# Optimization experiments

Measured on AMD Instinct MI355X. Metric: run time of the kernel, lower is better.

Reference implementation:

```python
import jax, jax.numpy as jnp
import numpy as np
from jax import lax

NEG = -1e9
B, H, C, TX, TY = 4, 256, 80, 256, 1024  # batch, hidden, mel bins, text len, mel len


def setup_inputs() -> dict:
    key = jax.random.key(0)
    k = jax.random.split(key, 6)
    en = jax.random.normal(k[0], (B, H, TX), jnp.float32)
    mu = jax.random.normal(k[1], (B, C, TX), jnp.float32)
    log_sigma = 0.1 * jax.random.normal(k[2], (B, C, TX), jnp.float32)
    y = jax.random.normal(k[3], (B, C, TY), jnp.float32)
    x_lengths = jax.random.randint(k[4], (B,), TX // 2, TX + 1, jnp.int32)
    y_lengths = jax.random.randint(k[5], (B,), TY // 2, TY + 1, jnp.int32)
    return {"en": en, "mu": mu, "log_sigma": log_sigma, "y": y,
            "x_lengths": x_lengths, "y_lengths": y_lengths}


def sequence_mask(lengths, max_len):
    return jnp.arange(max_len)[None, :] < lengths[:, None]


def compute_log_probs(mu, log_sigma, y):
    # y: [B,C,Ty] -> [B,1,Ty,C]; mu/log_sigma: [B,C,Tx] -> [B,Tx,1,C]
    yb = jnp.transpose(y, (0, 2, 1))[:, None]
    mub = jnp.transpose(mu, (0, 2, 1))[:, :, None]
    lsb = jnp.transpose(log_sigma, (0, 2, 1))[:, :, None]
    # mse / sigma^2 = (y-mu)^2 * exp(-2*log_sigma); mean over channel dim
    expo = -0.5 * jnp.mean((yb - mub) ** 2 * jnp.exp(-2.0 * lsb), axis=-1)  # [B,Tx,Ty]
    return expo - 0.5 * jnp.mean(lsb, axis=-1)  # broadcast [B,Tx,1] -> [B,Tx,Ty]


def maximum_path(logp, mask, x_lengths, y_lengths):
    """Monotonic alignment search (Glow-TTS Viterbi DP), vectorized over batch."""
    b, tx, ty = logp.shape
    lp = jnp.where(mask > 0, logp, NEG)
    cols = jnp.moveaxis(lp, 2, 0)  # [Ty, B, Tx]
    v0 = jnp.broadcast_to(jnp.where(jnp.arange(tx) == 0, 0.0, NEG), (b, tx)).astype(logp.dtype)

    def fwd(v, col):
        v_shift = jnp.concatenate([jnp.full((b, 1), NEG, v.dtype), v[:, :-1]], axis=1)
        diag = v_shift > v  # come from (x-1, y-1) rather than (x, y-1)
        return col + jnp.maximum(v, v_shift), diag

    _, diags = lax.scan(fwd, v0, cols)  # diags: [Ty, B, Tx] bool

    xs_idx = jnp.arange(tx)

    def bwd(idx, inp):
        yv, dcol = inp
        active = yv < y_lengths  # [B]
        row = (xs_idx[None, :] == idx[:, None]) & active[:, None]
        d = jnp.take_along_axis(dcol, idx[:, None], axis=1)[:, 0]
        idx = jnp.where(active & (idx > 0) & d, idx - 1, idx)
        return idx, row

    _, rows = lax.scan(bwd, x_lengths - 1, (jnp.arange(ty), diags), reverse=True)
    return lax.stop_gradient(jnp.moveaxis(rows, 0, 2).astype(logp.dtype))  # [B,Tx,Ty]


def generate_path(dr, mask):
    # dr: [B,Tx] durations; mask: [B,Tx,Ty]
    ty = mask.shape[-1]
    cum = jnp.cumsum(dr, axis=1)
    pm = (jnp.arange(ty)[None, None, :] < cum[:, :, None]).astype(dr.dtype)
    path = pm - jnp.pad(pm, ((0, 0), (1, 0), (0, 0)))[:, :-1]
    return path * mask


def reference(en, mu, log_sigma, y, x_lengths, y_lengths):
    tx, ty = mu.shape[-1], y.shape[-1]
    x_mask = sequence_mask(x_lengths, tx).astype(jnp.float32)  # [B,Tx]
    y_mask = sequence_mask(y_lengths, ty).astype(jnp.float32)  # [B,Ty]
    attn_mask = x_mask[:, :, None] * y_mask[:, None, :]        # [B,Tx,Ty]
    logp = compute_log_probs(mu, log_sigma, y)
    attn = maximum_path(logp, attn_mask, x_lengths, y_lengths)
    dr_mas = jnp.sum(attn, axis=-1)                            # durations [B,Tx]
    path = generate_path(dr_mas, attn_mask)                    # convert_dr_to_align
    # expand_encoder_outputs: attn^T @ en^T -> [B,H,Ty]
    o_en_ex = jnp.einsum('bxy,bhx->bhy', path, en)
    return o_en_ex, logp, attn, dr_mas
```

## Files before the change

### kernel.cpp

```cpp
#include <hip/hip_runtime.h>
#include <cstdint>
#include <cmath>

#define B_ 4
#define H_ 256
#define C_ 80
#define TX_ 256
#define TY_ 1024
#define NEGF (-1e9f)

#define OFF_LOGP (B_*H_*TY_)
#define OFF_ATTN (OFF_LOGP + B_*TX_*TY_)
#define OFF_DR   (OFF_ATTN + B_*TX_*TY_)

__global__ __launch_bounds__(256) void k_logp(
    const float* __restrict__ mu, const float* __restrict__ ls,
    const float* __restrict__ y, const int* __restrict__ xlp,
    const int* __restrict__ ylp, float* __restrict__ logp_out,
    float* __restrict__ lpT)
{
  const int b  = blockIdx.z;
  const int tq = blockIdx.y;
  const int x0 = blockIdx.x * 4;
  const int tid = threadIdx.x;
  const int lane = tid & 63;
  const int xi = tid >> 6;

  __shared__ double2 s_wm[4][C_];
  __shared__ double  s_wm2[4][C_];
  __shared__ double  s_lsv[4][C_];
  __shared__ double  s_K[4];
  __shared__ double  s_t0[4];
  __shared__ float   tile[256][4];

  for (int i = tid; i < 4 * C_; i += 256) {
    int xj = i / C_, c = i - xj * C_;
    double m = (double)mu[(b * C_ + c) * TX_ + x0 + xj];
    double l = (double)ls[(b * C_ + c) * TX_ + x0 + xj];
    double w = exp(-2.0 * l);
    s_wm[xj][c]  = make_double2(w, -2.0 * w * m);
    s_wm2[xj][c] = w * m * m;
    s_lsv[xj][c] = l;
  }
  __syncthreads();
  {
    int cc = lane;
    double kp = (cc < C_) ? s_wm2[xi][cc] : 0.0;
    double tp = (cc < C_) ? s_lsv[xi][cc] : 0.0;
    if (cc + 64 < C_) { kp += s_wm2[xi][cc + 64]; tp += s_lsv[xi][cc + 64]; }
#pragma unroll
    for (int off = 32; off; off >>= 1) {
      kp += __shfl_down(kp, off);
      tp += __shfl_down(tp, off);
    }
    if (cc == 0) { s_K[xi] = kp; s_t0[xi] = -0.5 * (tp * (1.0 / C_)); }
  }
  __syncthreads();

  double acc[4];
#pragma unroll
  for (int k = 0; k < 4; ++k) acc[k] = 0.0;

  const float4* yp = (const float4*)(y + (size_t)b * C_ * TY_ + tq * 256) + lane;
#pragma unroll 4
  for (int c = 0; c < C_; ++c) {
    float4 yv = yp[c * (TY_ / 4)];
    double y0 = yv.x, y1 = yv.y, y2 = yv.z, y3 = yv.w;
    double2 wm = s_wm[xi][c];
    double w = wm.x, m1 = wm.y;
    double u0 = fma(w, y0, m1), u1 = fma(w, y1, m1);
    double u2 = fma(w, y2, m1), u3 = fma(w, y3, m1);
    acc[0] = fma(u0, y0, acc[0]);
    acc[1] = fma(u1, y1, acc[1]);
    acc[2] = fma(u2, y2, acc[2]);
    acc[3] = fma(u3, y3, acc[3]);
  }

  const int xlen = xlp[b], ylen = ylp[b];
  const int x  = x0 + xi;
  const int t0 = tq * 256 + lane * 4;
  {
    double c0 = s_t0[xi], K = s_K[xi];
    float r[4];
#pragma unroll
    for (int k = 0; k < 4; ++k)
      r[k] = (float)((acc[k] + K) * (-0.5 / C_) + c0);
    *(float4*)&logp_out[((size_t)(b * TX_ + x)) * TY_ + t0] =
        make_float4(r[0], r[1], r[2], r[3]);
    bool xm = x < xlen;
#pragma unroll
    for (int k = 0; k < 4; ++k)
      tile[lane * 4 + k][xi] = (xm && (t0 + k) < ylen) ? r[k] : NEGF;
  }
  __syncthreads();

  float* dst = lpT + (size_t)b * TY_ * TX_ + x0;
  const float4* tp = (const float4*)tile;
  *(float4*)&dst[(size_t)(tq * 256 + tid) * TX_] = tp[tid];
}

#define POLL_PAIR(i)                                                     \
  { const volatile unsigned long long* vp2 =                             \
        (const volatile unsigned long long*)&flags[i];                   \
    for (;;) { unsigned long long fv = *vp2;                             \
      if ((unsigned)fv && (fv >> 32)) break;                             \
      __builtin_amdgcn_s_sleep(1); }                                     \
    asm volatile("" ::: "memory"); }

#define ISSUE8(BANK, SC, HALF)                                           \
  _Pragma("unroll")                                                      \
  for (int i = 0; i < 8; ++i)                                            \
    BANK[i] = ring4[(SC) * 1024 + ((HALF) * 8 + i) * 64 + lane];

#define CONS8(BANK)                                                      \
  _Pragma("unroll")                                                      \
  for (int u = 0; u < 8; ++u) {                                          \
    float4 col = BANK[u];                                                \
    sh_i = __builtin_amdgcn_update_dpp(sh_i, __float_as_int(v3),         \
                                       0x138, 0xf, 0xf, false);          \
    float sh = __int_as_float(sh_i);                                     \
    float m0 = fmaxf(v0, sh);                                            \
    float m1 = fmaxf(v1, v0);                                            \
    float m2 = fmaxf(v2, v1);                                            \
    float m3 = fmaxf(v3, v2);                                            \
    w0 = (w0 >> 1) | (__float_as_uint(v0 - m0) & 0x80000000u);           \
    w1 = (w1 >> 1) | (__float_as_uint(v1 - m1) & 0x80000000u);           \
    w2 = (w2 >> 1) | (__float_as_uint(v2 - m2) & 0x80000000u);           \
    w3 = (w3 >> 1) | (__float_as_uint(v3 - m3) & 0x80000000u);           \
    v0 = col.x + m0;                                                     \
    v1 = col.y + m1;                                                     \
    v2 = col.z + m2;                                                     \
    v3 = col.w + m3;                                                     \
  }

__global__ __launch_bounds__(256, 1) void k_dp(
    const float* __restrict__ lpT, const int* __restrict__ xlp,
    const int* __restrict__ ylp, float* __restrict__ dr_out,
    int* __restrict__ cum_ws, int* __restrict__ xt_ws)
{
  const int b = blockIdx.x;
  const int tid = threadIdx.x;
  const int lane = tid & 63;
  const int w = tid >> 6;
  __shared__ __align__(16) float    ring[6 * 16 * 256];
  __shared__ __align__(16) uint32_t bits[8192];
  __shared__ __align__(16) uint32_t dur[TX_];
  __shared__ __align__(16) uint32_t flags[64];
  __shared__ int      prog;

  const float4* gb4   = (const float4*)(lpT + (size_t)b * TY_ * TX_);
  const float4* ring4 = (const float4*)ring;

  const int ylen = ylp[b];
  const int nch  = ((ylen + 31) >> 5) << 1;

  if (tid < 64) flags[tid] = 0u;
  if (tid == 0) prog = -1;
  __syncthreads();

  if (w == 0) {
    volatile int* vprog = &prog;
    POLL_PAIR(0);
    float4 rrA[8], rrB[8];

    float v0 = (lane == 0) ? 0.0f : NEGF;
    float v1 = NEGF, v2 = NEGF, v3 = NEGF;
    uint32_t w0 = 0, w1 = 0, w2 = 0, w3 = 0;
    int sh_i = __float_as_int(NEGF);
    int slot = 0;

    ISSUE8(rrA, 0, 0);

    for (int cp = 0; cp < nch; cp += 2) {
      if (cp + 2 < nch) POLL_PAIR(cp + 2);
      const int s0 = slot;
      const int s1 = (s0 + 1 == 6) ? 0 : s0 + 1;
      const int s2 = (s1 + 1 == 6) ? 0 : s1 + 1;

      ISSUE8(rrB, s0, 1)
      CONS8(rrA)
      ISSUE8(rrA, s1, 0)
      CONS8(rrB)
      ISSUE8(rrB, s1, 1)
      CONS8(rrA)
      if (cp + 2 < nch) { ISSUE8(rrA, s2, 0) }
      CONS8(rrB)

      *(uint4*)&bits[(cp >> 1) * 256 + 4 * lane] = make_uint4(w0, w1, w2, w3);
      w0 = w1 = w2 = w3 = 0;
      asm volatile("" ::: "memory");
      *vprog = cp + 1;
      slot = s2;
    }
  } else {
    const int p = w - 1;
    volatile int*      vprog = &prog;
    volatile uint32_t* vflag = flags;
    for (int c = p; c < nch; c += 3) {
      const int need = c - 6;
      while (*vprog < need) __builtin_amdgcn_s_sleep(8);
      asm volatile("" ::: "memory");
      const float4* src = gb4 + (size_t)(c * 16) * 64 + lane;
      float4 tmp[16];
#pragma unroll
      for (int r = 0; r < 16; ++r) tmp[r] = src[r * 64];
      float4* dst = (float4*)&ring[(c % 6) * 4096] + lane;
#pragma unroll
      for (int r = 0; r < 16; ++r) dst[r * 64] = tmp[r];
      asm volatile("s_waitcnt lgkmcnt(0)" ::: "memory");
      vflag[c] = 1u;
    }
  }

  __syncthreads();
  dur[tid] = 0;
  __syncthreads();

  const int xlen = xlp[b];
  if (tid == 0) {
    int idx = xlen - 1;
    int t = ylen - 1;
    while (t >= 0) {
      if (idx == 0) { dur[0] = (uint32_t)(t + 1); break; }
      int ww = t >> 5, rrm = t & 31;
      uint32_t wd = bits[ww * 256 + idx];
      wd &= (rrm == 31) ? 0xffffffffu : ((1u << (rrm + 1)) - 1u);
      while (wd == 0 && ww > 0) { --ww; wd = bits[ww * 256 + idx]; }
      if (wd == 0) { dur[idx] = (uint32_t)(t + 1); break; }
      int bitpos = 31 - __builtin_clz(wd);
      int tp = (ww << 5) | bitpos;
      dur[idx] = (uint32_t)(t - tp + 1);
      --idx;
      t = tp - 1;
    }
  }
  __syncthreads();

  if (w == 0) {
    uint32_t d0 = dur[4 * lane], d1 = dur[4 * lane + 1];
    uint32_t d2 = dur[4 * lane + 2], d3 = dur[4 * lane + 3];
    uint32_t own = d0 + d1 + d2 + d3;
    uint32_t s = own;
#pragma unroll
    for (int off = 1; off < 64; off <<= 1) {
      uint32_t n = __shfl_up(s, off);
      if (lane >= off) s += n;
    }
    uint32_t base = s - own;
    uint32_t c0 = base + d0, c1 = c0 + d1, c2 = c1 + d2, c3 = c2 + d3;
    int x = 4 * lane;
    cum_ws[b * TX_ + x]     = (int)c0;
    cum_ws[b * TX_ + x + 1] = (int)c1;
    cum_ws[b * TX_ + x + 2] = (int)c2;
    cum_ws[b * TX_ + x + 3] = (int)c3;
    dr_out[b * TX_ + x]     = (float)d0;
    dr_out[b * TX_ + x + 1] = (float)d1;
    dr_out[b * TX_ + x + 2] = (float)d2;
    dr_out[b * TX_ + x + 3] = (float)d3;
    int* xt = xt_ws + b * TY_;
    for (uint32_t t = c0 - d0; t < c0; ++t) xt[t] = x;
    for (uint32_t t = c1 - d1; t < c1; ++t) xt[t] = x + 1;
    for (uint32_t t = c2 - d2; t < c2; ++t) xt[t] = x + 2;
    for (uint32_t t = c3 - d3; t < c3; ++t) xt[t] = x + 3;
  }
}

__global__ __launch_bounds__(256) void k_epi(
    const int* __restrict__ cum_ws, const int* __restrict__ xt_ws,
    const float* __restrict__ en, const int* __restrict__ ylp,
    float* __restrict__ attn, float* __restrict__ oen)
{
  const int b = blockIdx.y, bx = blockIdx.x, tid = threadIdx.x;
  __shared__ float row[TX_];
  if (bx < TX_) {
    const int x = bx;
    int hi = cum_ws[b * TX_ + x];
    int lo = (x > 0) ? cum_ws[b * TX_ + x - 1] : 0;
    int t0 = tid * 4;
    float4 v;
    v.x = (t0     >= lo && t0     < hi) ? 1.f : 0.f;
    v.y = (t0 + 1 >= lo && t0 + 1 < hi) ? 1.f : 0.f;
    v.z = (t0 + 2 >= lo && t0 + 2 < hi) ? 1.f : 0.f;
    v.w = (t0 + 3 >= lo && t0 + 3 < hi) ? 1.f : 0.f;
    *(float4*)&attn[((size_t)(b * TX_ + x)) * TY_ + t0] = v;
  } else {
    const int h = bx - TX_;
    row[tid] = en[((size_t)(b * H_ + h)) * TX_ + tid];
    __syncthreads();
    const int ylen = ylp[b];
    int t0 = tid * 4;
    int4 xi = *(const int4*)&xt_ws[b * TY_ + t0];
    float4 v;
    v.x = (t0     < ylen) ? row[xi.x & (TX_ - 1)] : 0.f;
    v.y = (t0 + 1 < ylen) ? row[xi.y & (TX_ - 1)] : 0.f;
    v.z = (t0 + 2 < ylen) ? row[xi.z & (TX_ - 1)] : 0.f;
    v.w = (t0 + 3 < ylen) ? row[xi.w & (TX_ - 1)] : 0.f;
    *(float4*)&oen[((size_t)(b * H_ + h)) * TY_ + t0] = v;
  }
}

extern "C" void kernel_launch(void* const* d_in, const int* in_sizes, int n_in,
                              void* d_out, int out_size, void* d_ws, size_t ws_size,
                              hipStream_t stream)
{
  const float* en = (const float*)d_in[0];
  const float* mu = (const float*)d_in[1];
  const float* ls = (const float*)d_in[2];
  const float* y  = (const float*)d_in[3];
  const int*   xl = (const int*)d_in[4];
  const int*   yl = (const int*)d_in[5];

  float* out  = (float*)d_out;
  float* oen  = out;
  float* logp = out + OFF_LOGP;
  float* attn = out + OFF_ATTN;
  float* dr   = out + OFF_DR;

  int* cum = (int*)d_ws;
  int* xt  = cum + B_ * TX_;

  k_logp<<<dim3(TX_ / 4, TY_ / 256, B_), 256, 0, stream>>>(mu, ls, y, xl, yl, logp, attn);
  k_dp  <<<B_,                           256, 0, stream>>>(attn, xl, yl, dr, cum, xt);
  k_epi <<<dim3(TX_ + H_, B_),           256, 0, stream>>>(cum, xt, en, yl, attn, oen);
}
```

Baseline: 163.6 us.

## Split Viterbi DP across two wavefronts with LDS boundary handoff

```diff
diff --git a/kernel.cpp b/kernel.cpp
--- a/kernel.cpp
+++ b/kernel.cpp
@@ -107,30 +107,42 @@
       __builtin_amdgcn_s_sleep(1); }                                     \
     asm volatile("" ::: "memory"); }
 
-#define ISSUE8(BANK, SC, HALF)                                           \
+#define ISSUE8W(BANK, SC, HALF, XOFF)                                    \
   _Pragma("unroll")                                                      \
   for (int i = 0; i < 8; ++i)                                            \
-    BANK[i] = ring4[(SC) * 1024 + ((HALF) * 8 + i) * 64 + lane];
-
-#define CONS8(BANK)                                                      \
+    BANK[i] = ring2[(SC) * 2048 + ((HALF) * 8 + i) * 128 + (XOFF) + lane];
+
+#define CONS8_W0(BANK, TB)                                               \
   _Pragma("unroll")                                                      \
   for (int u = 0; u < 8; ++u) {                                          \
-    float4 col = BANK[u];                                                \
-    sh_i = __builtin_amdgcn_update_dpp(sh_i, __float_as_int(v3),         \
+    float2 col = BANK[u];                                                \
+    sh_i = __builtin_amdgcn_update_dpp(sh_i, __float_as_int(v1),         \
                                        0x138, 0xf, 0xf, false);          \
     float sh = __int_as_float(sh_i);                                     \
     float m0 = fmaxf(v0, sh);                                            \
     float m1 = fmaxf(v1, v0);                                            \
-    float m2 = fmaxf(v2, v1);                                            \
-    float m3 = fmaxf(v3, v2);                                            \
     w0 = (w0 >> 1) | (__float_as_uint(v0 - m0) & 0x80000000u);           \
     w1 = (w1 >> 1) | (__float_as_uint(v1 - m1) & 0x80000000u);           \
-    w2 = (w2 >> 1) | (__float_as_uint(v2 - m2) & 0x80000000u);           \
-    w3 = (w3 >> 1) | (__float_as_uint(v3 - m3) & 0x80000000u);           \
     v0 = col.x + m0;                                                     \
     v1 = col.y + m1;                                                     \
-    v2 = col.z + m2;                                                     \
-    v3 = col.w + m3;                                                     \
+    { float* wr = (lane == 63) ? &bnd[(TB) + u] : &dummy2[lane];         \
+      *wr = v1; }                                                        \
+  }
+
+#define CONS8_W1(BANK, BI)                                               \
+  _Pragma("unroll")                                                      \
+  for (int u = 0; u < 8; ++u) {                                          \
+    float2 col = BANK[u];                                                \
+    sh_i = __builtin_amdgcn_update_dpp(sh_i, __float_as_int(v1),         \
+                                       0x138, 0xf, 0xf, false);          \
+    float sh = __int_as_float(sh_i);                                     \
+    if (lane == 0) sh = bv[(BI) + u];                                    \
+    float m0 = fmaxf(v0, sh);                                            \
+    float m1 = fmaxf(v1, v0);                                            \
+    w0 = (w0 >> 1) | (__float_as_uint(v0 - m0) & 0x80000000u);           \
+    w1 = (w1 >> 1) | (__float_as_uint(v1 - m1) & 0x80000000u);           \
+    v0 = col.x + m0;                                                     \
+    v1 = col.y + m1;                                                     \
   }
 
 __global__ __launch_bounds__(256, 1) void k_dp(
@@ -146,30 +158,72 @@
   __shared__ __align__(16) uint32_t bits[8192];
   __shared__ __align__(16) uint32_t dur[TX_];
   __shared__ __align__(16) uint32_t flags[64];
-  __shared__ int      prog;
+  __shared__ __align__(16) float    bnd[64];
+  __shared__ __align__(16) float    dummy2[64];
+  __shared__ int sprog0;
+  __shared__ int sprog1;
+  __shared__ int spgate;
 
   const float4* gb4   = (const float4*)(lpT + (size_t)b * TY_ * TX_);
-  const float4* ring4 = (const float4*)ring;
+  const float2* ring2 = (const float2*)ring;
 
   const int ylen = ylp[b];
   const int nch  = ((ylen + 31) >> 5) << 1;
 
-  if (tid < 64) flags[tid] = 0u;
-  if (tid == 0) prog = -1;
+  if (tid < 64) { flags[tid] = 0u; bnd[tid] = NEGF; }
+  if (tid == 0) { sprog0 = -1; sprog1 = -1; spgate = -1; }
   __syncthreads();
 
   if (w == 0) {
-    volatile int* vprog = &prog;
+    volatile int* vprog1 = &sprog1;
     POLL_PAIR(0);
-    float4 rrA[8], rrB[8];
-
+    float2 rrA[8], rrB[8];
     float v0 = (lane == 0) ? 0.0f : NEGF;
-    float v1 = NEGF, v2 = NEGF, v3 = NEGF;
-    uint32_t w0 = 0, w1 = 0, w2 = 0, w3 = 0;
+    float v1 = NEGF;
+    uint32_t w0 = 0, w1 = 0;
     int sh_i = __float_as_int(NEGF);
     int slot = 0;
 
-    ISSUE8(rrA, 0, 0);
+    ISSUE8W(rrA, 0, 0, 0)
+
+    for (int cp = 0; cp < nch; cp += 2) {
+      if (cp + 2 < nch) POLL_PAIR(cp + 2);
+      while (*vprog1 < cp - 3) __builtin_amdgcn_s_sleep(1);
+      asm volatile("" ::: "memory");
+      const int s0 = slot;
+      const int s1 = (s0 + 1 == 6) ? 0 : s0 + 1;
+      const int s2 = (s1 + 1 == 6) ? 0 : s1 + 1;
+      const int tb0 = (cp << 4) & 63;
+      const int tb1 = ((cp + 1) << 4) & 63;
+
+      ISSUE8W(rrB, s0, 1, 0)
+      CONS8_W0(rrA, tb0)
+      ISSUE8W(rrA, s1, 0, 0)
+      CONS8_W0(rrB, tb0 + 8)
+      asm volatile("" ::: "memory");
+      if (lane == 0) *(volatile int*)&sprog0 = cp;
+
+      ISSUE8W(rrB, s1, 1, 0)
+      CONS8_W0(rrA, tb1)
+      if (cp + 2 < nch) { ISSUE8W(rrA, s2, 0, 0) }
+      CONS8_W0(rrB, tb1 + 8)
+      *(uint2*)&bits[(cp >> 1) * 256 + 2 * lane] = make_uint2(w0, w1);
+      w0 = w1 = 0;
+      asm volatile("" ::: "memory");
+      if (lane == 0) *(volatile int*)&sprog0 = cp + 1;
+      slot = s2;
+    }
+  } else if (w == 1) {
+    volatile int* vprog0 = &sprog0;
+    POLL_PAIR(0);
+    float2 rrA[8], rrB[8];
+    float v0 = NEGF, v1 = NEGF;
+    uint32_t w0 = 0, w1 = 0;
+    int sh_i = __float_as_int(NEGF);
+    int slot = 0;
+    float bv[16];
+
+    ISSUE8W(rrA, 0, 0, 64)
 
     for (int cp = 0; cp < nch; cp += 2) {
       if (cp + 2 < nch) POLL_PAIR(cp + 2);
@@ -177,28 +231,43 @@
       const int s1 = (s0 + 1 == 6) ? 0 : s0 + 1;
       const int s2 = (s1 + 1 == 6) ? 0 : s1 + 1;
 
-      ISSUE8(rrB, s0, 1)
-      CONS8(rrA)
-      ISSUE8(rrA, s1, 0)
-      CONS8(rrB)
-      ISSUE8(rrB, s1, 1)
-      CONS8(rrA)
-      if (cp + 2 < nch) { ISSUE8(rrA, s2, 0) }
-      CONS8(rrB)
-
-      *(uint4*)&bits[(cp >> 1) * 256 + 4 * lane] = make_uint4(w0, w1, w2, w3);
-      w0 = w1 = w2 = w3 = 0;
-      asm volatile("" ::: "memory");
-      *vprog = cp + 1;
+      while (*vprog0 < cp) __builtin_amdgcn_s_sleep(1);
+      asm volatile("" ::: "memory");
+      { const int base = (cp << 4) - 1;
+#pragma unroll
+        for (int i = 0; i < 16; ++i) bv[i] = bnd[(base + i) & 63]; }
+      ISSUE8W(rrB, s0, 1, 64)
+      CONS8_W1(rrA, 0)
+      ISSUE8W(rrA, s1, 0, 64)
+      CONS8_W1(rrB, 8)
+      asm volatile("" ::: "memory");
+      if (lane == 0) *(volatile int*)&sprog1 = cp;
+
+      while (*vprog0 < cp + 1) __builtin_amdgcn_s_sleep(1);
+      asm volatile("" ::: "memory");
+      { const int base = ((cp + 1) << 4) - 1;
+#pragma unroll
+        for (int i = 0; i < 16; ++i) bv[i] = bnd[(base + i) & 63]; }
+      ISSUE8W(rrB, s1, 1, 64)
+      CONS8_W1(rrA, 0)
+      if (cp + 2 < nch) { ISSUE8W(rrA, s2, 0, 64) }
+      CONS8_W1(rrB, 8)
+      *(uint2*)&bits[(cp >> 1) * 256 + 128 + 2 * lane] = make_uint2(w0, w1);
+      w0 = w1 = 0;
+      asm volatile("" ::: "memory");
+      if (lane == 0) {
+        *(volatile int*)&sprog1 = cp + 1;
+        *(volatile int*)&spgate = cp + 1;
+      }
       slot = s2;
     }
   } else {
-    const int p = w - 1;
-    volatile int*      vprog = &prog;
+    const int p = w - 2;
+    volatile int*      vgate = &spgate;
     volatile uint32_t* vflag = flags;
-    for (int c = p; c < nch; c += 3) {
+    for (int c = p; c < nch; c += 2) {
       const int need = c - 6;
-      while (*vprog < need) __builtin_amdgcn_s_sleep(8);
+      while (*vgate < need) __builtin_amdgcn_s_sleep(8);
       asm volatile("" ::: "memory");
       const float4* src = gb4 + (size_t)(c * 16) * 64 + lane;
       float4 tmp[16];
```

Result: no change. 165.2 us (+1.0%).
